# Optimization experiments

Hardware: AMD Instinct MI355X
Metric: run time of the kernel (lower is better)

## Reference

```python
import jax, jax.numpy as jnp
import numpy as np

KERNEL_SIZE = (8,)

def setup_inputs() -> dict:
    key = jax.random.key(0)
    k1, = jax.random.split(key, 1)
    inputs = jax.random.normal(k1, (32, 131072, 8), dtype=jnp.float32)
    w = jnp.ones(KERNEL_SIZE, dtype=jnp.float32)  # initializer='ones', non-trainable
    return {"inputs": inputs, "w": w}

def reference(inputs, w):
    # keys[b, n] = sum_c inputs[b, n, c] * w[c]
    keys = jnp.einsum('bnc,c->bn', inputs, w)
    idx = jnp.argsort(keys, axis=-1)                     # [B, N] int
    # batched gather: out[b, i, :] = inputs[b, idx[b, i], :]
    out = jnp.take_along_axis(inputs, idx[:, :, None], axis=1)
    return out
```

## Files before the change

### kernel.cpp

```cpp
#include <hip/hip_runtime.h>


#define NB    32
#define NPB   131072
#define NK    (NB * NPB)
#define TPB   256
#define EPT   16
#define EPB   (TPB * EPT)
#define BPB   (NPB / EPB)
#define NBLK  (NB * BPB)
#define BINS  256
#define PBINS 65536
#define BCAP  1024
#define BEPT  4

typedef unsigned long long u64;
typedef unsigned int u32;
typedef unsigned short u16;
typedef unsigned char u8;

__device__ __forceinline__ u32 fkey(float x) {
    u32 u = __float_as_uint(x);
    return u ^ ((u & 0x80000000u) ? 0xFFFFFFFFu : 0x80000000u);
}

__device__ __forceinline__ float seqdot(float4 a, float4 c,
                                        float w0, float w1, float w2, float w3,
                                        float w4, float w5, float w6, float w7) {
    float k = __fmul_rn(a.x, w0);
    k = __fadd_rn(k, __fmul_rn(a.y, w1));
    k = __fadd_rn(k, __fmul_rn(a.z, w2));
    k = __fadd_rn(k, __fmul_rn(a.w, w3));
    k = __fadd_rn(k, __fmul_rn(c.x, w4));
    k = __fadd_rn(k, __fmul_rn(c.y, w5));
    k = __fadd_rn(k, __fmul_rn(c.z, w6));
    k = __fadd_rn(k, __fmul_rn(c.w, w7));
    return k;
}

__device__ __forceinline__ u64 matchany(u32 d) {
    u64 m = ~0ull;
    #pragma unroll
    for (int k = 0; k < 8; ++k) {
        u64 bk = __ballot((d >> k) & 1u);
        m &= ((d >> k) & 1u) ? bk : ~bk;
    }
    return m;
}

__global__ void mapgen(u8* __restrict__ map8)
{
    int p = blockIdx.x * TPB + threadIdx.x;
    u32 lo = (u32)p << 16;
    u32 u = (lo & 0x80000000u) ? (lo ^ 0x80000000u) : ~lo;
    float x = __uint_as_float(u);
    int bkt;
    if (x != x) {
        bkt = (lo & 0x80000000u) ? 255 : 0;
    } else {
        double cdf = 0.5 * (1.0 + erf((double)x * 0.25));
        bkt = (int)(cdf * 256.0);
        if (bkt > 255) bkt = 255;
        if (bkt < 0) bkt = 0;
    }
    map8[p] = (u8)bkt;
}

__global__ void khist0f(const float* __restrict__ in, const float* __restrict__ w,
                        const u8* __restrict__ map8, u32* __restrict__ keys,
                        u32* __restrict__ hist)
{
    __shared__ u32 h[BINS];
    int t = threadIdx.x;
    h[t] = 0;
    __syncthreads();
    int b = blockIdx.x / BPB, blk = blockIdx.x % BPB;
    size_t base = (size_t)b * NPB + (size_t)blk * EPB;
    int lane = t & 63;
    float w0 = w[0], w1 = w[1], w2 = w[2], w3 = w[3];
    float w4 = w[4], w5 = w[5], w6 = w[6], w7 = w[7];
    #pragma unroll
    for (int i = 0; i < EPT; ++i) {
        size_t row = base + t + i * TPB;
        const float4* p = (const float4*)in + row * 2;
        float4 a = p[0], c = p[1];
        u32 fk = fkey(seqdot(a, c, w0, w1, w2, w3, w4, w5, w6, w7));
        keys[row] = fk;
        u32 d = map8[fk >> 16];
        u64 m = matchany(d);
        if (lane == __ffsll(m) - 1) atomicAdd(&h[d], (u32)__popcll(m));
    }
    __syncthreads();
    hist[(b * BINS + t) * BPB + blk] = h[t];
}

__global__ void rscan(u32* __restrict__ hist)
{
    int b = blockIdx.x, t = threadIdx.x;
    u32* H = hist + b * BINS * BPB;
    u32 v[32], s = 0;
    #pragma unroll
    for (int k = 0; k < 32; ++k) { v[k] = H[t * 32 + k]; s += v[k]; }
    int lane = t & 63, wid = t >> 6;
    u32 inc = s;
    #pragma unroll
    for (int off = 1; off < 64; off <<= 1) {
        u32 y = __shfl_up(inc, off, 64);
        if (lane >= off) inc += y;
    }
    __shared__ u32 wsum[4];
    if (lane == 63) wsum[wid] = inc;
    __syncthreads();
    u32 wo = 0;
    #pragma unroll
    for (int wI = 0; wI < 4; ++wI) if (wI < wid) wo += wsum[wI];
    u32 run = wo + inc - s;
    #pragma unroll
    for (int k = 0; k < 32; ++k) { u32 c = v[k]; H[t * 32 + k] = run; run += c; }
}

__launch_bounds__(TPB, 4)
__global__ void scatA(const float* __restrict__ in, const u32* __restrict__ keys,
                      const u8* __restrict__ map8, float* __restrict__ out,
                      const u32* __restrict__ hist)
{
    __shared__ u32 s_pack[EPB];
    __shared__ u32 s_wcnt[4][BINS];
    __shared__ u32 s_dbase[BINS];
    __shared__ u32 s_gbase[BINS];
    __shared__ u32 s_wsum[4];
    int t = threadIdx.x, lane = t & 63, wid = t >> 6;
    int b = blockIdx.x / BPB, blk = blockIdx.x % BPB;
    const float4* inw = (const float4*)in + ((size_t)b * NPB + (size_t)blk * EPB) * 2;
    const u32* kw = keys + (size_t)b * NPB + (size_t)blk * EPB;
    const u8* M = map8;

    #pragma unroll
    for (int k = 0; k < 4; ++k) ((u32*)s_wcnt)[t + k * TPB] = 0;
    __syncthreads();

    u32 dgt[EPT];
    u32 rnk[EPT];
    #pragma unroll
    for (int i = 0; i < EPT; ++i) {
        u32 k = kw[wid * 1024 + i * 64 + lane];
        dgt[i] = M[k >> 16];
    }

    #pragma unroll
    for (int i = 0; i < EPT; ++i) {
        u32 d = dgt[i];
        u64 m = matchany(d);
        int leader = __ffsll(m) - 1;
        u32 baseCnt = 0;
        if (lane == leader) {
            baseCnt = s_wcnt[wid][d];
            s_wcnt[wid][d] = baseCnt + (u32)__popcll(m);
        }
        baseCnt = __shfl(baseCnt, leader, 64);
        rnk[i] = baseCnt + (u32)__popcll(m & ((1ull << lane) - 1ull));
        __builtin_amdgcn_wave_barrier();
    }
    __syncthreads();

    u32 c0 = s_wcnt[0][t], c1 = s_wcnt[1][t], c2 = s_wcnt[2][t], c3 = s_wcnt[3][t];
    u32 tot = c0 + c1 + c2 + c3;
    s_wcnt[0][t] = 0; s_wcnt[1][t] = c0; s_wcnt[2][t] = c0 + c1; s_wcnt[3][t] = c0 + c1 + c2;
    u32 inc = tot;
    #pragma unroll
    for (int off = 1; off < 64; off <<= 1) {
        u32 y = __shfl_up(inc, off, 64);
        if (lane >= off) inc += y;
    }
    if (lane == 63) s_wsum[wid] = inc;
    __syncthreads();
    u32 wo = 0;
    #pragma unroll
    for (int wI = 0; wI < 4; ++wI) if (wI < wid) wo += s_wsum[wI];
    s_dbase[t] = wo + inc - tot;
    s_gbase[t] = hist[(b * BINS + t) * BPB + blk];
    __syncthreads();

    #pragma unroll
    for (int i = 0; i < EPT; ++i) {
        u32 d = dgt[i];
        u32 pos = s_dbase[d] + s_wcnt[wid][d] + rnk[i];
        u32 srcpos = (u32)(wid * 1024 + i * 64 + lane);
        s_pack[pos] = (d << 12) | srcpos;
    }
    __syncthreads();

    float4* outb = (float4*)out + ((size_t)b << 18);
    #pragma unroll
    for (int i = 0; i < EPT; ++i) {
        int j = i * TPB + t;
        u32 pack = s_pack[j];
        u32 d = pack >> 12;
        u32 sp = pack & 4095u;
        u32 gpos = s_gbase[d] + (u32)j - s_dbase[d];
        float4 x = inw[2 * sp], y = inw[2 * sp + 1];
        float4* dr = outb + (size_t)gpos * 2;
        dr[0] = x; dr[1] = y;
    }
}

__launch_bounds__(TPB, 3)
__global__ void sortB(float* __restrict__ data, const float* __restrict__ w,
                      const u32* __restrict__ hist)
{
    __shared__ float4 s_rows[BCAP * 2];
    __shared__ u32 s_keyA[BCAP];
    __shared__ u32 s_keyB[BCAP];
    __shared__ u16 s_posA[BCAP];
    __shared__ u16 s_posB[BCAP];
    __shared__ u32 s_wcnt[4][BINS];
    __shared__ u32 s_dbase[BINS];
    __shared__ u32 s_wsum[4];
    __shared__ u32 s_mn[4], s_mx[4];

    int b = blockIdx.x >> 8;
    int bk = blockIdx.x & 255;
    u32 start = hist[(b * BINS + bk) * BPB];
    u32 end   = (bk == 255) ? (u32)NPB : hist[(b * BINS + bk + 1) * BPB];
    u32 cnt = end - start;
    if (cnt == 0) return;
    if (cnt > BCAP) cnt = BCAP;

    int t = threadIdx.x, lane = t & 63, wid = t >> 6;
    float4* base4 = (float4*)data + ((size_t)b * NPB + start) * 2;

    for (u32 j = t; j < cnt * 2; j += TPB) s_rows[j] = base4[j];
    __syncthreads();

    float w0 = w[0], w1 = w[1], w2 = w[2], w3 = w[3];
    float w4 = w[4], w5 = w[5], w6 = w[6], w7 = w[7];
    u32 kmin = 0xFFFFFFFFu, kmax = 0;
    for (u32 j = t; j < cnt; j += TPB) {
        float4 a = s_rows[2 * j], c = s_rows[2 * j + 1];
        u32 fk = fkey(seqdot(a, c, w0, w1, w2, w3, w4, w5, w6, w7));
        s_keyA[j] = fk;
        kmin = (fk < kmin) ? fk : kmin;
        kmax = (fk > kmax) ? fk : kmax;
    }
    #pragma unroll
    for (int off = 1; off < 64; off <<= 1) {
        u32 a = __shfl_xor(kmin, off, 64);
        u32 z = __shfl_xor(kmax, off, 64);
        kmin = (a < kmin) ? a : kmin;
        kmax = (z > kmax) ? z : kmax;
    }
    if (lane == 0) { s_mn[wid] = kmin; s_mx[wid] = kmax; }
    __syncthreads();
    kmin = s_mn[0]; kmax = s_mx[0];
    #pragma unroll
    for (int wI = 1; wI < 4; ++wI) {
        kmin = (s_mn[wI] < kmin) ? s_mn[wI] : kmin;
        kmax = (s_mx[wI] > kmax) ? s_mx[wI] : kmax;
    }
    u32 span = kmax - kmin;
    if (span == 0) return;

    for (u32 j = t; j < cnt; j += TPB) { s_keyA[j] -= kmin; s_posA[j] = (u16)j; }
    for (u32 j = cnt + t; j < BCAP; j += TPB) { s_keyA[j] = 0xFFFFFFFFu; s_posA[j] = (u16)j; }
    int npasses = (39 - __clz(span)) >> 3;

    u32* keyS = s_keyA; u32* keyD = s_keyB;
    u16* posS = s_posA; u16* posD = s_posB;

    for (int p = 0; p < npasses; ++p) {
        int sh = 8 * p;
        #pragma unroll
        for (int k = 0; k < 4; ++k) ((u32*)s_wcnt)[t + k * TPB] = 0;
        __syncthreads();

        u32 kk[BEPT], rr[BEPT], dd[BEPT];
        #pragma unroll
        for (int i = 0; i < BEPT; ++i) {
            int e = wid * 256 + i * 64 + lane;
            kk[i] = keyS[e];
            u32 dg = (kk[i] >> sh) & 255u;
            dd[i] = dg;
            u64 m = matchany(dg);
            int leader = __ffsll(m) - 1;
            u32 bc = 0;
            if (lane == leader) {
                bc = s_wcnt[wid][dg];
                s_wcnt[wid][dg] = bc + (u32)__popcll(m);
            }
            bc = __shfl(bc, leader, 64);
            rr[i] = bc + (u32)__popcll(m & ((1ull << lane) - 1ull));
            __builtin_amdgcn_wave_barrier();
        }
        __syncthreads();

        u32 c0 = s_wcnt[0][t], c1 = s_wcnt[1][t], c2 = s_wcnt[2][t], c3 = s_wcnt[3][t];
        u32 tot = c0 + c1 + c2 + c3;
        s_wcnt[0][t] = 0; s_wcnt[1][t] = c0; s_wcnt[2][t] = c0 + c1; s_wcnt[3][t] = c0 + c1 + c2;
        u32 inc = tot;
        #pragma unroll
        for (int off = 1; off < 64; off <<= 1) {
            u32 y = __shfl_up(inc, off, 64);
            if (lane >= off) inc += y;
        }
        if (lane == 63) s_wsum[wid] = inc;
        __syncthreads();
        u32 wo = 0;
        #pragma unroll
        for (int wI = 0; wI < 4; ++wI) if (wI < wid) wo += s_wsum[wI];
        s_dbase[t] = wo + inc - tot;
        __syncthreads();

        #pragma unroll
        for (int i = 0; i < BEPT; ++i) {
            int e = wid * 256 + i * 64 + lane;
            u32 dg = dd[i];
            u32 np = s_dbase[dg] + s_wcnt[wid][dg] + rr[i];
            keyD[np] = kk[i];
            posD[np] = posS[e];
        }
        __syncthreads();

        u32* tk = keyS; keyS = keyD; keyD = tk;
        u16* tp = posS; posS = posD; posD = tp;
    }

    for (u32 j = t; j < cnt; j += TPB) {
        u32 sp = posS[j];
        float4 x = s_rows[2 * sp], y = s_rows[2 * sp + 1];
        base4[2 * j] = x; base4[2 * j + 1] = y;
    }
}

extern "C" void kernel_launch(void* const* d_in, const int* in_sizes, int n_in,
                              void* d_out, int out_size, void* d_ws, size_t ws_size,
                              hipStream_t stream)
{
    const float* in = (const float*)d_in[0];
    const float* w  = (const float*)d_in[1];
    float* out = (float*)d_out;

    char* wsb = (char*)d_ws;
    u32* keys = (u32*)wsb;
    u32* hist = (u32*)(wsb + (size_t)NK * 4);
    u8*  map8 = (u8*) (wsb + (size_t)NK * 4 + (size_t)NB * BINS * BPB * 4);

    mapgen<<<PBINS / TPB, TPB, 0, stream>>>(map8);
    khist0f<<<NBLK, TPB, 0, stream>>>(in, w, map8, keys, hist);
    rscan<<<NB, TPB, 0, stream>>>(hist);
    scatA<<<NBLK, TPB, 0, stream>>>(in, keys, map8, out, hist);
    sortB<<<NB * BINS, TPB, 0, stream>>>(out, w, hist);
}
```

Before: 234.8 us.

## Recompute sort keys in scatter pass and drop LDS row staging in bucket sort

The histogram kernel no longer writes a per-row key buffer. The scatter kernel recomputes each key from the input rows instead, which removes a global key write and read at the cost of reading the input rows a second time. The bucket sort kernel no longer stages rows in shared memory: it computes keys straight from global memory and does the final permutation as a gather from global into registers, then a write-back. Dropping that shared-memory buffer lets it raise its launch bound from 3 to 4 blocks per SM, but the extra and uncoalesced global reads lean on L2 hits. A leftover stub scatA kernel remains but is never launched.

```diff
diff --git a/kernel.cpp b/kernel.cpp
--- a/kernel.cpp
+++ b/kernel.cpp
@@ -66,9 +66,8 @@
     map8[p] = (u8)bkt;
 }
 
-__global__ void khist0f(const float* __restrict__ in, const float* __restrict__ w,
-                        const u8* __restrict__ map8, u32* __restrict__ keys,
-                        u32* __restrict__ hist)
+__global__ void khist0(const float* __restrict__ in, const float* __restrict__ w,
+                       const u8* __restrict__ map8, u32* __restrict__ hist)
 {
     __shared__ u32 h[BINS];
     int t = threadIdx.x;
@@ -85,7 +84,6 @@
         const float4* p = (const float4*)in + row * 2;
         float4 a = p[0], c = p[1];
         u32 fk = fkey(seqdot(a, c, w0, w1, w2, w3, w4, w5, w6, w7));
-        keys[row] = fk;
         u32 d = map8[fk >> 16];
         u64 m = matchany(d);
         if (lane == __ffsll(m) - 1) atomicAdd(&h[d], (u32)__popcll(m));
@@ -120,9 +118,8 @@
 }
 
 __launch_bounds__(TPB, 4)
-__global__ void scatA(const float* __restrict__ in, const u32* __restrict__ keys,
-                      const u8* __restrict__ map8, float* __restrict__ out,
-                      const u32* __restrict__ hist)
+__global__ void scatA(const float* __restrict__ in, const u8* __restrict__ map8,
+                      float* __restrict__ out, const u32* __restrict__ hist)
 {
     __shared__ u32 s_pack[EPB];
     __shared__ u32 s_wcnt[4][BINS];
@@ -132,19 +129,70 @@
     int t = threadIdx.x, lane = t & 63, wid = t >> 6;
     int b = blockIdx.x / BPB, blk = blockIdx.x % BPB;
     const float4* inw = (const float4*)in + ((size_t)b * NPB + (size_t)blk * EPB) * 2;
-    const u32* kw = keys + (size_t)b * NPB + (size_t)blk * EPB;
     const u8* M = map8;
 
     #pragma unroll
     for (int k = 0; k < 4; ++k) ((u32*)s_wcnt)[t + k * TPB] = 0;
     __syncthreads();
+
+    float w0, w1, w2, w3, w4, w5, w6, w7;
+    {
+    }
 
     u32 dgt[EPT];
     u32 rnk[EPT];
     #pragma unroll
     for (int i = 0; i < EPT; ++i) {
-        u32 k = kw[wid * 1024 + i * 64 + lane];
-        dgt[i] = M[k >> 16];
+        int sp = wid * 1024 + i * 64 + lane;
+        float4 a = inw[2 * sp], c = inw[2 * sp + 1];
+        extern __shared__ u32 _dummy[];
+        u32 fk;
+        {
+            const float* wp = (const float*)s_gbase;
+            (void)wp;
+            fk = 0;
+        }
+        (void)a; (void)c; (void)fk;
+        dgt[i] = 0;
+    }
+    const float* wg = (const float*)((const void*)0);
+    (void)wg;
+    #pragma unroll
+    for (int i = 0; i < EPT; ++i) {
+    }
+    (void)dgt; (void)rnk; (void)M;
+}
+
+__launch_bounds__(TPB, 4)
+__global__ void scatA2(const float* __restrict__ in, const float* __restrict__ w,
+                       const u8* __restrict__ map8, float* __restrict__ out,
+                       const u32* __restrict__ hist)
+{
+    __shared__ u32 s_pack[EPB];
+    __shared__ u32 s_wcnt[4][BINS];
+    __shared__ u32 s_dbase[BINS];
+    __shared__ u32 s_gbase[BINS];
+    __shared__ u32 s_wsum[4];
+    int t = threadIdx.x, lane = t & 63, wid = t >> 6;
+    int b = blockIdx.x / BPB, blk = blockIdx.x % BPB;
+    const float4* inw = (const float4*)in + ((size_t)b * NPB + (size_t)blk * EPB) * 2;
+    const u8* M = map8;
+
+    #pragma unroll
+    for (int k = 0; k < 4; ++k) ((u32*)s_wcnt)[t + k * TPB] = 0;
+    __syncthreads();
+
+    float w0 = w[0], w1 = w[1], w2 = w[2], w3 = w[3];
+    float w4 = w[4], w5 = w[5], w6 = w[6], w7 = w[7];
+
+    u32 dgt[EPT];
+    u32 rnk[EPT];
+    #pragma unroll
+    for (int i = 0; i < EPT; ++i) {
+        int sp = wid * 1024 + i * 64 + lane;
+        float4 a = inw[2 * sp], c = inw[2 * sp + 1];
+        u32 fk = fkey(seqdot(a, c, w0, w1, w2, w3, w4, w5, w6, w7));
+        dgt[i] = M[fk >> 16];
     }
 
     #pragma unroll
@@ -204,11 +252,10 @@
     }
 }
 
-__launch_bounds__(TPB, 3)
+__launch_bounds__(TPB, 4)
 __global__ void sortB(float* __restrict__ data, const float* __restrict__ w,
                       const u32* __restrict__ hist)
 {
-    __shared__ float4 s_rows[BCAP * 2];
     __shared__ u32 s_keyA[BCAP];
     __shared__ u32 s_keyB[BCAP];
     __shared__ u16 s_posA[BCAP];
@@ -229,19 +276,18 @@
     int t = threadIdx.x, lane = t & 63, wid = t >> 6;
     float4* base4 = (float4*)data + ((size_t)b * NPB + start) * 2;
 
-    for (u32 j = t; j < cnt * 2; j += TPB) s_rows[j] = base4[j];
-    __syncthreads();
-
     float w0 = w[0], w1 = w[1], w2 = w[2], w3 = w[3];
     float w4 = w[4], w5 = w[5], w6 = w[6], w7 = w[7];
     u32 kmin = 0xFFFFFFFFu, kmax = 0;
     for (u32 j = t; j < cnt; j += TPB) {
-        float4 a = s_rows[2 * j], c = s_rows[2 * j + 1];
+        float4 a = base4[2 * j], c = base4[2 * j + 1];
         u32 fk = fkey(seqdot(a, c, w0, w1, w2, w3, w4, w5, w6, w7));
         s_keyA[j] = fk;
+        s_posA[j] = (u16)j;
         kmin = (fk < kmin) ? fk : kmin;
         kmax = (fk > kmax) ? fk : kmax;
     }
+    for (u32 j = cnt + t; j < BCAP; j += TPB) { s_keyA[j] = 0xFFFFFFFFu; s_posA[j] = (u16)j; }
     #pragma unroll
     for (int off = 1; off < 64; off <<= 1) {
         u32 a = __shfl_xor(kmin, off, 64);
@@ -260,8 +306,8 @@
     u32 span = kmax - kmin;
     if (span == 0) return;
 
-    for (u32 j = t; j < cnt; j += TPB) { s_keyA[j] -= kmin; s_posA[j] = (u16)j; }
-    for (u32 j = cnt + t; j < BCAP; j += TPB) { s_keyA[j] = 0xFFFFFFFFu; s_posA[j] = (u16)j; }
+    for (u32 j = t; j < cnt; j += TPB) s_keyA[j] -= kmin;
+    __syncthreads();
     int npasses = (39 - __clz(span)) >> 3;
 
     u32* keyS = s_keyA; u32* keyD = s_keyB;
@@ -324,10 +370,24 @@
         u16* tp = posS; posS = posD; posD = tp;
     }
 
-    for (u32 j = t; j < cnt; j += TPB) {
-        u32 sp = posS[j];
-        float4 x = s_rows[2 * sp], y = s_rows[2 * sp + 1];
-        base4[2 * j] = x; base4[2 * j + 1] = y;
+    float4 rx[BEPT], ry[BEPT];
+    #pragma unroll
+    for (int i = 0; i < BEPT; ++i) {
+        u32 j = (u32)t + (u32)i * TPB;
+        if (j < cnt) {
+            u32 sp = posS[j];
+            rx[i] = base4[2 * sp];
+            ry[i] = base4[2 * sp + 1];
+        }
+    }
+    __syncthreads();
+    #pragma unroll
+    for (int i = 0; i < BEPT; ++i) {
+        u32 j = (u32)t + (u32)i * TPB;
+        if (j < cnt) {
+            base4[2 * j] = rx[i];
+            base4[2 * j + 1] = ry[i];
+        }
     }
 }
 
@@ -340,13 +400,12 @@
     float* out = (float*)d_out;
 
     char* wsb = (char*)d_ws;
-    u32* keys = (u32*)wsb;
-    u32* hist = (u32*)(wsb + (size_t)NK * 4);
-    u8*  map8 = (u8*) (wsb + (size_t)NK * 4 + (size_t)NB * BINS * BPB * 4);
+    u32* hist = (u32*)wsb;
+    u8*  map8 = (u8*)(wsb + (size_t)NB * BINS * BPB * 4);
 
     mapgen<<<PBINS / TPB, TPB, 0, stream>>>(map8);
-    khist0f<<<NBLK, TPB, 0, stream>>>(in, w, map8, keys, hist);
+    khist0<<<NBLK, TPB, 0, stream>>>(in, w, map8, hist);
     rscan<<<NB, TPB, 0, stream>>>(hist);
-    scatA<<<NBLK, TPB, 0, stream>>>(in, keys, map8, out, hist);
+    scatA2<<<NBLK, TPB, 0, stream>>>(in, w, map8, out, hist);
     sortB<<<NB * BINS, TPB, 0, stream>>>(out, w, hist);
 }
```

Result: slower. 262.2 us (+11.7%).

## Recompute keys in scatter pass and rank buckets by all-pairs counting

Applied to the files above, without the earlier changes.

The histogram kernel no longer writes a global keys buffer. The scatter kernel instead recomputes each key from the input rows, trading a global key write and read for a second read of the input rows, which should mostly hit in cache. The per-bucket multi-pass LDS radix sort is replaced by a rank-by-counting sort. Each thread keeps up to four rows in registers, compares their (key, index) pair against every key in the bucket held in shared memory, and writes each row straight to its rank. This removes the radix passes, their barriers and the large shared staging buffers, raising occupancy, but the compare work grows quadratically with bucket size.

```diff
diff --git a/kernel.cpp b/kernel.cpp
--- a/kernel.cpp
+++ b/kernel.cpp
@@ -12,11 +12,10 @@
 #define BINS  256
 #define PBINS 65536
 #define BCAP  1024
-#define BEPT  4
+#define RPT   4
 
 typedef unsigned long long u64;
 typedef unsigned int u32;
-typedef unsigned short u16;
 typedef unsigned char u8;
 
 __device__ __forceinline__ u32 fkey(float x) {
@@ -66,9 +65,8 @@
     map8[p] = (u8)bkt;
 }
 
-__global__ void khist0f(const float* __restrict__ in, const float* __restrict__ w,
-                        const u8* __restrict__ map8, u32* __restrict__ keys,
-                        u32* __restrict__ hist)
+__global__ void khist0(const float* __restrict__ in, const float* __restrict__ w,
+                       const u8* __restrict__ map8, u32* __restrict__ hist)
 {
     __shared__ u32 h[BINS];
     int t = threadIdx.x;
@@ -85,7 +83,6 @@
         const float4* p = (const float4*)in + row * 2;
         float4 a = p[0], c = p[1];
         u32 fk = fkey(seqdot(a, c, w0, w1, w2, w3, w4, w5, w6, w7));
-        keys[row] = fk;
         u32 d = map8[fk >> 16];
         u64 m = matchany(d);
         if (lane == __ffsll(m) - 1) atomicAdd(&h[d], (u32)__popcll(m));
@@ -120,9 +117,9 @@
 }
 
 __launch_bounds__(TPB, 4)
-__global__ void scatA(const float* __restrict__ in, const u32* __restrict__ keys,
-                      const u8* __restrict__ map8, float* __restrict__ out,
-                      const u32* __restrict__ hist)
+__global__ void scatA2(const float* __restrict__ in, const float* __restrict__ w,
+                       const u8* __restrict__ map8, float* __restrict__ out,
+                       const u32* __restrict__ hist)
 {
     __shared__ u32 s_pack[EPB];
     __shared__ u32 s_wcnt[4][BINS];
@@ -132,19 +129,23 @@
     int t = threadIdx.x, lane = t & 63, wid = t >> 6;
     int b = blockIdx.x / BPB, blk = blockIdx.x % BPB;
     const float4* inw = (const float4*)in + ((size_t)b * NPB + (size_t)blk * EPB) * 2;
-    const u32* kw = keys + (size_t)b * NPB + (size_t)blk * EPB;
     const u8* M = map8;
 
     #pragma unroll
     for (int k = 0; k < 4; ++k) ((u32*)s_wcnt)[t + k * TPB] = 0;
     __syncthreads();
+
+    float w0 = w[0], w1 = w[1], w2 = w[2], w3 = w[3];
+    float w4 = w[4], w5 = w[5], w6 = w[6], w7 = w[7];
 
     u32 dgt[EPT];
     u32 rnk[EPT];
     #pragma unroll
     for (int i = 0; i < EPT; ++i) {
-        u32 k = kw[wid * 1024 + i * 64 + lane];
-        dgt[i] = M[k >> 16];
+        int sp = wid * 1024 + i * 64 + lane;
+        float4 a = inw[2 * sp], c = inw[2 * sp + 1];
+        u32 fk = fkey(seqdot(a, c, w0, w1, w2, w3, w4, w5, w6, w7));
+        dgt[i] = M[fk >> 16];
     }
 
     #pragma unroll
@@ -204,19 +205,11 @@
     }
 }
 
-__launch_bounds__(TPB, 3)
+__launch_bounds__(TPB, 4)
 __global__ void sortB(float* __restrict__ data, const float* __restrict__ w,
                       const u32* __restrict__ hist)
 {
-    __shared__ float4 s_rows[BCAP * 2];
-    __shared__ u32 s_keyA[BCAP];
-    __shared__ u32 s_keyB[BCAP];
-    __shared__ u16 s_posA[BCAP];
-    __shared__ u16 s_posB[BCAP];
-    __shared__ u32 s_wcnt[4][BINS];
-    __shared__ u32 s_dbase[BINS];
-    __shared__ u32 s_wsum[4];
-    __shared__ u32 s_mn[4], s_mx[4];
+    __shared__ u32 s_key[BCAP];
 
     int b = blockIdx.x >> 8;
     int bk = blockIdx.x & 255;
@@ -226,108 +219,44 @@
     if (cnt == 0) return;
     if (cnt > BCAP) cnt = BCAP;
 
-    int t = threadIdx.x, lane = t & 63, wid = t >> 6;
+    int t = threadIdx.x;
     float4* base4 = (float4*)data + ((size_t)b * NPB + start) * 2;
-
-    for (u32 j = t; j < cnt * 2; j += TPB) s_rows[j] = base4[j];
-    __syncthreads();
 
     float w0 = w[0], w1 = w[1], w2 = w[2], w3 = w[3];
     float w4 = w[4], w5 = w[5], w6 = w[6], w7 = w[7];
-    u32 kmin = 0xFFFFFFFFu, kmax = 0;
-    for (u32 j = t; j < cnt; j += TPB) {
-        float4 a = s_rows[2 * j], c = s_rows[2 * j + 1];
-        u32 fk = fkey(seqdot(a, c, w0, w1, w2, w3, w4, w5, w6, w7));
-        s_keyA[j] = fk;
-        kmin = (fk < kmin) ? fk : kmin;
-        kmax = (fk > kmax) ? fk : kmax;
-    }
-    #pragma unroll
-    for (int off = 1; off < 64; off <<= 1) {
-        u32 a = __shfl_xor(kmin, off, 64);
-        u32 z = __shfl_xor(kmax, off, 64);
-        kmin = (a < kmin) ? a : kmin;
-        kmax = (z > kmax) ? z : kmax;
-    }
-    if (lane == 0) { s_mn[wid] = kmin; s_mx[wid] = kmax; }
-    __syncthreads();
-    kmin = s_mn[0]; kmax = s_mx[0];
-    #pragma unroll
-    for (int wI = 1; wI < 4; ++wI) {
-        kmin = (s_mn[wI] < kmin) ? s_mn[wI] : kmin;
-        kmax = (s_mx[wI] > kmax) ? s_mx[wI] : kmax;
-    }
-    u32 span = kmax - kmin;
-    if (span == 0) return;
-
-    for (u32 j = t; j < cnt; j += TPB) { s_keyA[j] -= kmin; s_posA[j] = (u16)j; }
-    for (u32 j = cnt + t; j < BCAP; j += TPB) { s_keyA[j] = 0xFFFFFFFFu; s_posA[j] = (u16)j; }
-    int npasses = (39 - __clz(span)) >> 3;
-
-    u32* keyS = s_keyA; u32* keyD = s_keyB;
-    u16* posS = s_posA; u16* posD = s_posB;
-
-    for (int p = 0; p < npasses; ++p) {
-        int sh = 8 * p;
+
+    float4 rx[RPT], ry[RPT];
+    u64 me[RPT];
+    #pragma unroll
+    for (int k = 0; k < RPT; ++k) {
+        u32 j = (u32)t + (u32)k * TPB;
+        me[k] = ~0ull;
+        if (j < cnt) {
+            rx[k] = base4[2 * j];
+            ry[k] = base4[2 * j + 1];
+            u32 fk = fkey(seqdot(rx[k], ry[k], w0, w1, w2, w3, w4, w5, w6, w7));
+            s_key[j] = fk;
+            me[k] = ((u64)fk << 10) | (u64)j;
+        }
+    }
+    __syncthreads();
+
+    u32 rnk[RPT] = {0, 0, 0, 0};
+    for (u32 j = 0; j < cnt; ++j) {
+        u64 cj = ((u64)s_key[j] << 10) | (u64)j;
         #pragma unroll
-        for (int k = 0; k < 4; ++k) ((u32*)s_wcnt)[t + k * TPB] = 0;
-        __syncthreads();
-
-        u32 kk[BEPT], rr[BEPT], dd[BEPT];
-        #pragma unroll
-        for (int i = 0; i < BEPT; ++i) {
-            int e = wid * 256 + i * 64 + lane;
-            kk[i] = keyS[e];
-            u32 dg = (kk[i] >> sh) & 255u;
-            dd[i] = dg;
-            u64 m = matchany(dg);
-            int leader = __ffsll(m) - 1;
-            u32 bc = 0;
-            if (lane == leader) {
-                bc = s_wcnt[wid][dg];
-                s_wcnt[wid][dg] = bc + (u32)__popcll(m);
-            }
-            bc = __shfl(bc, leader, 64);
-            rr[i] = bc + (u32)__popcll(m & ((1ull << lane) - 1ull));
-            __builtin_amdgcn_wave_barrier();
+        for (int k = 0; k < RPT; ++k)
+            rnk[k] += (cj < me[k]) ? 1u : 0u;
+    }
+
+    #pragma unroll
+    for (int k = 0; k < RPT; ++k) {
+        u32 j = (u32)t + (u32)k * TPB;
+        if (j < cnt) {
+            float4* dr = base4 + (size_t)rnk[k] * 2;
+            dr[0] = rx[k];
+            dr[1] = ry[k];
         }
-        __syncthreads();
-
-        u32 c0 = s_wcnt[0][t], c1 = s_wcnt[1][t], c2 = s_wcnt[2][t], c3 = s_wcnt[3][t];
-        u32 tot = c0 + c1 + c2 + c3;
-        s_wcnt[0][t] = 0; s_wcnt[1][t] = c0; s_wcnt[2][t] = c0 + c1; s_wcnt[3][t] = c0 + c1 + c2;
-        u32 inc = tot;
-        #pragma unroll
-        for (int off = 1; off < 64; off <<= 1) {
-            u32 y = __shfl_up(inc, off, 64);
-            if (lane >= off) inc += y;
-        }
-        if (lane == 63) s_wsum[wid] = inc;
-        __syncthreads();
-        u32 wo = 0;
-        #pragma unroll
-        for (int wI = 0; wI < 4; ++wI) if (wI < wid) wo += s_wsum[wI];
-        s_dbase[t] = wo + inc - tot;
-        __syncthreads();
-
-        #pragma unroll
-        for (int i = 0; i < BEPT; ++i) {
-            int e = wid * 256 + i * 64 + lane;
-            u32 dg = dd[i];
-            u32 np = s_dbase[dg] + s_wcnt[wid][dg] + rr[i];
-            keyD[np] = kk[i];
-            posD[np] = posS[e];
-        }
-        __syncthreads();
-
-        u32* tk = keyS; keyS = keyD; keyD = tk;
-        u16* tp = posS; posS = posD; posD = tp;
-    }
-
-    for (u32 j = t; j < cnt; j += TPB) {
-        u32 sp = posS[j];
-        float4 x = s_rows[2 * sp], y = s_rows[2 * sp + 1];
-        base4[2 * j] = x; base4[2 * j + 1] = y;
     }
 }
 
@@ -340,13 +269,12 @@
     float* out = (float*)d_out;
 
     char* wsb = (char*)d_ws;
-    u32* keys = (u32*)wsb;
-    u32* hist = (u32*)(wsb + (size_t)NK * 4);
-    u8*  map8 = (u8*) (wsb + (size_t)NK * 4 + (size_t)NB * BINS * BPB * 4);
+    u32* hist = (u32*)wsb;
+    u8*  map8 = (u8*)(wsb + (size_t)NB * BINS * BPB * 4);
 
     mapgen<<<PBINS / TPB, TPB, 0, stream>>>(map8);
-    khist0f<<<NBLK, TPB, 0, stream>>>(in, w, map8, keys, hist);
+    khist0<<<NBLK, TPB, 0, stream>>>(in, w, map8, hist);
     rscan<<<NB, TPB, 0, stream>>>(hist);
-    scatA<<<NBLK, TPB, 0, stream>>>(in, keys, map8, out, hist);
+    scatA2<<<NBLK, TPB, 0, stream>>>(in, w, map8, out, hist);
     sortB<<<NB * BINS, TPB, 0, stream>>>(out, w, hist);
 }
```

New measurement: 510.6 us. 2.17x slower.
